# Optimization experiments

Hardware: AMD Instinct MI355X
Metric: run time of the kernel (lower is better)

The kernel has to match this reference:

```python
import jax, jax.numpy as jnp
import numpy as np

EPS = 1e-12  # matches torch F.normalize eps

def _l2norm(x):
    n = jnp.linalg.norm(x, axis=-1, keepdims=True)
    return x / jnp.maximum(n, EPS)

def setup_inputs() -> dict:
    key = jax.random.key(0)
    k1, k2, k3, k4, k5 = jax.random.split(key, 5)
    B, S, D, V, N = 8, 512, 128, 100000, 2048
    query_embeddings = jax.random.normal(k1, (B, S, D), dtype=jnp.float32)
    key_embeddings = jax.random.normal(k2, (V, D), dtype=jnp.float32)
    batch_idx = jax.random.randint(k3, (N, 1), 0, B)
    seq_idx = jax.random.randint(k4, (N, 1), 0, S)
    label_locations = jnp.concatenate([batch_idx, seq_idx], axis=1).astype(jnp.int64)
    labels = jax.random.randint(k5, (N,), 0, V).astype(jnp.int64)
    return {"query_embeddings": query_embeddings, "key_embeddings": key_embeddings,
            "label_locations": label_locations, "labels": labels}

def reference(query_embeddings, key_embeddings, label_locations, labels):
    # gather supervised positions: [N, D]
    q = query_embeddings[label_locations[:, 0], label_locations[:, 1]]
    q = _l2norm(q)
    k = _l2norm(key_embeddings)
    logits = jnp.einsum('nd,vd->nv', q, k)  # [N, V]
    # mean-reduced softmax cross entropy
    logz = jax.nn.logsumexp(logits, axis=-1)  # [N]
    tgt = jnp.take_along_axis(logits, labels[:, None], axis=-1)[:, 0]
    return jnp.mean(logz - tgt)
```

## Files before the change

### kernel.cpp

```cpp
#include <hip/hip_runtime.h>
#include <hip/hip_bf16.h>

typedef __attribute__((ext_vector_type(8))) short short8;
typedef __attribute__((ext_vector_type(4))) short short4v;
typedef __attribute__((ext_vector_type(4))) float f32x4;

namespace {
constexpr int D    = 128;
constexpr int SEQ  = 512;
constexpr int NV   = 100000;
constexpr int NN   = 2048;
constexpr int KC   = 64;
constexpr int CHUNK_B = KC * D * 2;
constexpr int CPS     = 25;
constexpr int NSLICE  = 63;
constexpr int MBLKS   = 8;
constexpr int GRID    = MBLKS * NSLICE;
constexpr float LOG2E = 1.4426950408889634f;
constexpr float EPSN  = 1e-12f;
}

__global__ __launch_bounds__(256)
void prep_kernel(const float* __restrict__ qemb,
                 const float* __restrict__ kemb,
                 const int*   __restrict__ loc,
                 const int*   __restrict__ labels,
                 __hip_bfloat16* __restrict__ Kn,
                 __hip_bfloat16* __restrict__ Qn,
                 float* __restrict__ tgt,
                 float* __restrict__ sums,
                 unsigned int* __restrict__ counter)
{
    const int gid = blockIdx.x * blockDim.x + threadIdx.x;
    if (gid < NN) sums[gid] = 0.f;
    if (gid == NN) *counter = 0u;

    const int gw   = gid >> 6;
    const int lane = threadIdx.x & 63;
    const int half = lane >> 5;
    const int l32  = lane & 31;
    const int row  = gw * 2 + half;
    if (row >= NV + NN) return;

    if (row < NV) {
        const float* src = kemb + (size_t)row * D;
        float4 v = *(const float4*)(src + l32 * 4);
        float ss = v.x * v.x + v.y * v.y + v.z * v.z + v.w * v.w;
        #pragma unroll
        for (int m = 1; m < 32; m <<= 1) ss += __shfl_xor(ss, m);
        float inv = 1.0f / fmaxf(sqrtf(ss), EPSN);
        union { __hip_bfloat162 h2[2]; short4v s4; } u;
        u.h2[0].x = __float2bfloat16(v.x * inv);
        u.h2[0].y = __float2bfloat16(v.y * inv);
        u.h2[1].x = __float2bfloat16(v.z * inv);
        u.h2[1].y = __float2bfloat16(v.w * inv);
        *(short4v*)((char*)(Kn + (size_t)row * D) + l32 * 8) = u.s4;
    } else {
        const int n = row - NV;
        const int b = loc[2 * n], s = loc[2 * n + 1];
        const float* q = qemb + ((size_t)b * SEQ + s) * D;
        const float* k = kemb + (size_t)labels[n] * D;
        float4 qv = *(const float4*)(q + l32 * 4);
        float4 kv = *(const float4*)(k + l32 * 4);
        float qq = qv.x * qv.x + qv.y * qv.y + qv.z * qv.z + qv.w * qv.w;
        float kk = kv.x * kv.x + kv.y * kv.y + kv.z * kv.z + kv.w * kv.w;
        float qk = qv.x * kv.x + qv.y * kv.y + qv.z * kv.z + qv.w * kv.w;
        #pragma unroll
        for (int m = 1; m < 32; m <<= 1) {
            qq += __shfl_xor(qq, m);
            kk += __shfl_xor(kk, m);
            qk += __shfl_xor(qk, m);
        }
        float invq = 1.0f / fmaxf(sqrtf(qq), EPSN);
        float scl  = LOG2E * invq;
        union { __hip_bfloat162 h2[2]; short4v s4; } u;
        u.h2[0].x = __float2bfloat16(qv.x * scl);
        u.h2[0].y = __float2bfloat16(qv.y * scl);
        u.h2[1].x = __float2bfloat16(qv.z * scl);
        u.h2[1].y = __float2bfloat16(qv.w * scl);
        *(short4v*)((char*)(Qn + (size_t)n * D) + l32 * 8) = u.s4;
        if (l32 == 0)
            tgt[n] = qk * invq / fmaxf(sqrtf(kk), EPSN);
    }
}

__global__ __launch_bounds__(256, 2)
void lse_main(const __hip_bfloat16* __restrict__ Kn,
              const __hip_bfloat16* __restrict__ Qn,
              const float* __restrict__ tgt,
              float* __restrict__ sums,
              unsigned int* __restrict__ counter,
              float* __restrict__ out)
{
    __shared__ char lds[4 * CHUNK_B];
    const int tid  = threadIdx.x;
    const int lane = tid & 63;
    const int lr   = lane & 15;
    const int lh   = lane >> 4;
    const int w    = tid >> 6;

    const int bid = blockIdx.x;
    const int lin = (bid & 7) * NSLICE + (bid >> 3);
    const int slice = lin >> 3;
    const int mblk  = lin & 7;

    const int chunk0 = slice * CPS;
    const int m0 = mblk * 256 + w * 64;
    const char* kbase = (const char*)Kn;

    auto stage = [&](int c, int bi) {
        const int keybase = (chunk0 + c) * KC;
        #pragma unroll
        for (int r = 0; r < 4; ++r) {
            const int i   = w * 4 + r;
            const int kic = i * 4 + lh;
            const int key = min(keybase + kic, NV - 1);
            const int sb  = (lr ^ (kic & 7)) << 4;
            const char* g = kbase + (size_t)key * 256 + sb;
            const char* l = lds + bi * CHUNK_B + i * 1024;
            __builtin_amdgcn_global_load_lds(
                (const __attribute__((address_space(1))) void*)g,
                (__attribute__((address_space(3))) void*)l, 16, 0, 0);
        }
    };

    stage(0, 0); stage(1, 1); stage(2, 2);

    short8 qf[4][4];
    #pragma unroll
    for (int rg = 0; rg < 4; ++rg)
        #pragma unroll
        for (int ds = 0; ds < 4; ++ds)
            qf[rg][ds] = *(const short8*)((const short*)Qn +
                          (size_t)(m0 + rg * 16 + lr) * D + ds * 32 + lh * 8);

    float rowsum[4][4] = {};
    __syncthreads();

    for (int c = 0; c < CPS; ++c) {
        if (c + 3 < CPS) stage(c + 3, (c + 3) & 3);

        const char* buf = lds + (c & 3) * CHUNK_B;
        const int vbase = (chunk0 + c) * KC;
        const bool full = (vbase + KC <= NV);
        #pragma unroll
        for (int kg = 0; kg < 4; ++kg) {
            const int kic = kg * 16 + lr;
            const int rx  = (kic & 7) << 4;
            f32x4 acc[4] = {{0,0,0,0},{0,0,0,0},{0,0,0,0},{0,0,0,0}};
            #pragma unroll
            for (int ds2 = 0; ds2 < 4; ++ds2) {
                short8 bf = *(const short8*)(buf +
                              ((kic * 256 + ds2 * 64 + lh * 16) ^ rx));
                #pragma unroll
                for (int rg = 0; rg < 4; ++rg)
                    acc[rg] = __builtin_amdgcn_mfma_f32_16x16x32_bf16(
                                  qf[rg][ds2], bf, acc[rg], 0, 0, 0);
            }
            if (full) {
                #pragma unroll
                for (int rg = 0; rg < 4; ++rg)
                    #pragma unroll
                    for (int j = 0; j < 4; ++j)
                        rowsum[rg][j] += __builtin_amdgcn_exp2f(acc[rg][j]);
            } else {
                const bool ok = (vbase + kic) < NV;
                #pragma unroll
                for (int rg = 0; rg < 4; ++rg)
                    #pragma unroll
                    for (int j = 0; j < 4; ++j)
                        rowsum[rg][j] += ok ? __builtin_amdgcn_exp2f(acc[rg][j]) : 0.f;
            }
        }
        if (c < CPS - 3) {
            asm volatile("s_waitcnt vmcnt(8)" ::: "memory");
            __builtin_amdgcn_s_barrier();
            asm volatile("" ::: "memory");
        } else if (c == CPS - 3) {
            asm volatile("s_waitcnt vmcnt(4)" ::: "memory");
            __builtin_amdgcn_s_barrier();
            asm volatile("" ::: "memory");
        } else if (c == CPS - 2) {
            asm volatile("s_waitcnt vmcnt(0)" ::: "memory");
            __builtin_amdgcn_s_barrier();
            asm volatile("" ::: "memory");
        }
    }

    #pragma unroll
    for (int rg = 0; rg < 4; ++rg)
        #pragma unroll
        for (int j = 0; j < 4; ++j) {
            float v = rowsum[rg][j];
            v += __shfl_xor(v, 1);
            v += __shfl_xor(v, 2);
            v += __shfl_xor(v, 4);
            v += __shfl_xor(v, 8);
            if (lr == 0)
                atomicAdd(&sums[m0 + rg * 16 + lh * 4 + j], v);
        }

    __threadfence();
    __syncthreads();
    __shared__ int ticket_s;
    if (tid == 0) ticket_s = (int)atomicAdd(counter, 1u);
    __syncthreads();
    if (ticket_s == GRID - 1) {
        __threadfence();
        __shared__ float wsum[4];
        float acc = 0.f;
        for (int n = tid; n < NN; n += 256) {
            float sv = __hip_atomic_load(&sums[n], __ATOMIC_RELAXED,
                                         __HIP_MEMORY_SCOPE_AGENT);
            acc += logf(sv) - tgt[n];
        }
        #pragma unroll
        for (int m = 1; m < 64; m <<= 1) acc += __shfl_xor(acc, m);
        if ((tid & 63) == 0) wsum[tid >> 6] = acc;
        __syncthreads();
        if (tid == 0)
            out[0] = (wsum[0] + wsum[1] + wsum[2] + wsum[3]) / (float)NN;
    }
}

extern "C" void kernel_launch(void* const* d_in, const int* in_sizes, int n_in,
                              void* d_out, int out_size, void* d_ws, size_t ws_size,
                              hipStream_t stream)
{
    const float* qemb   = (const float*)d_in[0];
    const float* kemb   = (const float*)d_in[1];
    const int*   loc    = (const int*)d_in[2];
    const int*   labels = (const int*)d_in[3];
    float* out = (float*)d_out;

    char* ws = (char*)d_ws;
    __hip_bfloat16* Kn = (__hip_bfloat16*)ws;
    size_t off = (size_t)NV * D * 2;
    __hip_bfloat16* Qn = (__hip_bfloat16*)(ws + off);
    off += (size_t)NN * D * 2;
    float* sums = (float*)(ws + off); off += (size_t)NN * 4;
    float* tgt  = (float*)(ws + off); off += (size_t)NN * 4;
    unsigned int* counter = (unsigned int*)(ws + off);

    {
        int waves  = (NV + NN + 1) / 2;
        int blocks = (waves + 3) / 4;
        prep_kernel<<<blocks, 256, 0, stream>>>(qemb, kemb, loc, labels,
                                                Kn, Qn, tgt, sums, counter);
    }
    lse_main<<<GRID, 256, 0, stream>>>(Kn, Qn, tgt, sums, counter, out);
}
```

Baseline: 186.1 us.

## Widen LSE blocks to 512 threads, interleave key chunks, grid-stride prep

The main kernel now uses 512-thread blocks covering 512 query rows each, so four M-blocks replace eight and each staged key chunk is reused by twice as many queries. Key chunks are assigned to slices with a stride of NSLICE instead of contiguously, and the block-to-XCD mapping is rebalanced for the uneven 500-block grid. The prep kernel switches to a fixed 2048-block grid-stride loop. The aim is to halve K reloads from L2/HBM. The risk is that `launch_bounds(512,4)` caps VGPRs tightly while the Q fragments alone need many registers, which could cause spills.

```diff
diff --git a/kernel.cpp b/kernel.cpp
--- a/kernel.cpp
+++ b/kernel.cpp
@@ -12,9 +12,10 @@
 constexpr int NN   = 2048;
 constexpr int KC   = 64;
 constexpr int CHUNK_B = KC * D * 2;
-constexpr int CPS     = 25;
-constexpr int NSLICE  = 63;
-constexpr int MBLKS   = 8;
+constexpr int NCHUNK  = 1563;
+constexpr int CPS     = 13;
+constexpr int NSLICE  = 125;
+constexpr int MBLKS   = 4;
 constexpr int GRID    = MBLKS * NSLICE;
 constexpr float LOG2E = 1.4426950408889634f;
 constexpr float EPSN  = 1e-12f;
@@ -31,60 +32,64 @@
                  float* __restrict__ sums,
                  unsigned int* __restrict__ counter)
 {
-    const int gid = blockIdx.x * blockDim.x + threadIdx.x;
-    if (gid < NN) sums[gid] = 0.f;
-    if (gid == NN) *counter = 0u;
-
-    const int gw   = gid >> 6;
-    const int lane = threadIdx.x & 63;
+    const int tid  = threadIdx.x;
+    const int gid0 = blockIdx.x * 256 + tid;
+    if (gid0 < NN) sums[gid0] = 0.f;
+    if (gid0 == NN) *counter = 0u;
+
+    const int lane = tid & 63;
     const int half = lane >> 5;
     const int l32  = lane & 31;
-    const int row  = gw * 2 + half;
-    if (row >= NV + NN) return;
-
-    if (row < NV) {
-        const float* src = kemb + (size_t)row * D;
-        float4 v = *(const float4*)(src + l32 * 4);
-        float ss = v.x * v.x + v.y * v.y + v.z * v.z + v.w * v.w;
-        #pragma unroll
-        for (int m = 1; m < 32; m <<= 1) ss += __shfl_xor(ss, m);
-        float inv = 1.0f / fmaxf(sqrtf(ss), EPSN);
-        union { __hip_bfloat162 h2[2]; short4v s4; } u;
-        u.h2[0].x = __float2bfloat16(v.x * inv);
-        u.h2[0].y = __float2bfloat16(v.y * inv);
-        u.h2[1].x = __float2bfloat16(v.z * inv);
-        u.h2[1].y = __float2bfloat16(v.w * inv);
-        *(short4v*)((char*)(Kn + (size_t)row * D) + l32 * 8) = u.s4;
-    } else {
-        const int n = row - NV;
-        const int b = loc[2 * n], s = loc[2 * n + 1];
-        const float* q = qemb + ((size_t)b * SEQ + s) * D;
-        const float* k = kemb + (size_t)labels[n] * D;
-        float4 qv = *(const float4*)(q + l32 * 4);
-        float4 kv = *(const float4*)(k + l32 * 4);
-        float qq = qv.x * qv.x + qv.y * qv.y + qv.z * qv.z + qv.w * qv.w;
-        float kk = kv.x * kv.x + kv.y * kv.y + kv.z * kv.z + kv.w * kv.w;
-        float qk = qv.x * kv.x + qv.y * kv.y + qv.z * kv.z + qv.w * kv.w;
-        #pragma unroll
-        for (int m = 1; m < 32; m <<= 1) {
-            qq += __shfl_xor(qq, m);
-            kk += __shfl_xor(kk, m);
-            qk += __shfl_xor(qk, m);
-        }
-        float invq = 1.0f / fmaxf(sqrtf(qq), EPSN);
-        float scl  = LOG2E * invq;
-        union { __hip_bfloat162 h2[2]; short4v s4; } u;
-        u.h2[0].x = __float2bfloat16(qv.x * scl);
-        u.h2[0].y = __float2bfloat16(qv.y * scl);
-        u.h2[1].x = __float2bfloat16(qv.z * scl);
-        u.h2[1].y = __float2bfloat16(qv.w * scl);
-        *(short4v*)((char*)(Qn + (size_t)n * D) + l32 * 8) = u.s4;
-        if (l32 == 0)
-            tgt[n] = qk * invq / fmaxf(sqrtf(kk), EPSN);
+    const int wv0  = gid0 >> 6;
+    const int nwv  = (gridDim.x * 256) >> 6;
+
+    for (int wv = wv0; wv * 2 < NV + NN; wv += nwv) {
+        const int row = wv * 2 + half;
+
+        if (row < NV) {
+            const float* src = kemb + (size_t)row * D;
+            float4 v = *(const float4*)(src + l32 * 4);
+            float ss = v.x * v.x + v.y * v.y + v.z * v.z + v.w * v.w;
+            #pragma unroll
+            for (int m = 1; m < 32; m <<= 1) ss += __shfl_xor(ss, m);
+            float inv = 1.0f / fmaxf(sqrtf(ss), EPSN);
+            union { __hip_bfloat162 h2[2]; short4v s4; } u;
+            u.h2[0].x = __float2bfloat16(v.x * inv);
+            u.h2[0].y = __float2bfloat16(v.y * inv);
+            u.h2[1].x = __float2bfloat16(v.z * inv);
+            u.h2[1].y = __float2bfloat16(v.w * inv);
+            *(short4v*)((char*)(Kn + (size_t)row * D) + l32 * 8) = u.s4;
+        } else {
+            const int n = row - NV;
+            const int b = loc[2 * n], s = loc[2 * n + 1];
+            const float* q = qemb + ((size_t)b * SEQ + s) * D;
+            const float* k = kemb + (size_t)labels[n] * D;
+            float4 qv = *(const float4*)(q + l32 * 4);
+            float4 kv = *(const float4*)(k + l32 * 4);
+            float qq = qv.x * qv.x + qv.y * qv.y + qv.z * qv.z + qv.w * qv.w;
+            float kk = kv.x * kv.x + kv.y * kv.y + kv.z * kv.z + kv.w * kv.w;
+            float qk = qv.x * kv.x + qv.y * kv.y + qv.z * kv.z + qv.w * kv.w;
+            #pragma unroll
+            for (int m = 1; m < 32; m <<= 1) {
+                qq += __shfl_xor(qq, m);
+                kk += __shfl_xor(kk, m);
+                qk += __shfl_xor(qk, m);
+            }
+            float invq = 1.0f / fmaxf(sqrtf(qq), EPSN);
+            float scl  = LOG2E * invq;
+            union { __hip_bfloat162 h2[2]; short4v s4; } u;
+            u.h2[0].x = __float2bfloat16(qv.x * scl);
+            u.h2[0].y = __float2bfloat16(qv.y * scl);
+            u.h2[1].x = __float2bfloat16(qv.z * scl);
+            u.h2[1].y = __float2bfloat16(qv.w * scl);
+            *(short4v*)((char*)(Qn + (size_t)n * D) + l32 * 8) = u.s4;
+            if (l32 == 0)
+                tgt[n] = qk * invq / fmaxf(sqrtf(kk), EPSN);
+        }
     }
 }
 
-__global__ __launch_bounds__(256, 2)
+__global__ __launch_bounds__(512, 4)
 void lse_main(const __hip_bfloat16* __restrict__ Kn,
               const __hip_bfloat16* __restrict__ Qn,
               const float* __restrict__ tgt,
@@ -100,19 +105,21 @@
     const int w    = tid >> 6;
 
     const int bid = blockIdx.x;
-    const int lin = (bid & 7) * NSLICE + (bid >> 3);
-    const int slice = lin >> 3;
-    const int mblk  = lin & 7;
-
-    const int chunk0 = slice * CPS;
-    const int m0 = mblk * 256 + w * 64;
+    const int xcd = bid & 7, idx = bid >> 3;
+    const int base = (xcd < 4) ? xcd * 63 : 252 + (xcd - 4) * 62;
+    const int lin  = base + idx;
+    const int slice = lin >> 2;
+    const int mblk  = lin & 3;
+
+    const int m0 = mblk * 512 + w * 64;
     const char* kbase = (const char*)Kn;
 
     auto stage = [&](int c, int bi) {
-        const int keybase = (chunk0 + c) * KC;
-        #pragma unroll
-        for (int r = 0; r < 4; ++r) {
-            const int i   = w * 4 + r;
+        const int chunk = slice + c * NSLICE;
+        const int keybase = chunk * KC;
+        #pragma unroll
+        for (int r = 0; r < 2; ++r) {
+            const int i   = w * 2 + r;
             const int kic = i * 4 + lh;
             const int key = min(keybase + kic, NV - 1);
             const int sb  = (lr ^ (kic & 7)) << 4;
@@ -141,7 +148,7 @@
         if (c + 3 < CPS) stage(c + 3, (c + 3) & 3);
 
         const char* buf = lds + (c & 3) * CHUNK_B;
-        const int vbase = (chunk0 + c) * KC;
+        const int vbase = (slice + c * NSLICE) * KC;
         const bool full = (vbase + KC <= NV);
         #pragma unroll
         for (int kg = 0; kg < 4; ++kg) {
@@ -173,11 +180,11 @@
             }
         }
         if (c < CPS - 3) {
-            asm volatile("s_waitcnt vmcnt(8)" ::: "memory");
+            asm volatile("s_waitcnt vmcnt(4)" ::: "memory");
             __builtin_amdgcn_s_barrier();
             asm volatile("" ::: "memory");
         } else if (c == CPS - 3) {
-            asm volatile("s_waitcnt vmcnt(4)" ::: "memory");
+            asm volatile("s_waitcnt vmcnt(2)" ::: "memory");
             __builtin_amdgcn_s_barrier();
             asm volatile("" ::: "memory");
         } else if (c == CPS - 2) {
@@ -207,9 +214,9 @@
     __syncthreads();
     if (ticket_s == GRID - 1) {
         __threadfence();
-        __shared__ float wsum[4];
+        __shared__ float wsum[8];
         float acc = 0.f;
-        for (int n = tid; n < NN; n += 256) {
+        for (int n = tid; n < NN; n += 512) {
             float sv = __hip_atomic_load(&sums[n], __ATOMIC_RELAXED,
                                          __HIP_MEMORY_SCOPE_AGENT);
             acc += logf(sv) - tgt[n];
@@ -218,8 +225,12 @@
         for (int m = 1; m < 64; m <<= 1) acc += __shfl_xor(acc, m);
         if ((tid & 63) == 0) wsum[tid >> 6] = acc;
         __syncthreads();
-        if (tid == 0)
-            out[0] = (wsum[0] + wsum[1] + wsum[2] + wsum[3]) / (float)NN;
+        if (tid == 0) {
+            float t = 0.f;
+            #pragma unroll
+            for (int i = 0; i < 8; ++i) t += wsum[i];
+            out[0] = t / (float)NN;
+        }
     }
 }
 
@@ -242,11 +253,7 @@
     float* tgt  = (float*)(ws + off); off += (size_t)NN * 4;
     unsigned int* counter = (unsigned int*)(ws + off);
 
-    {
-        int waves  = (NV + NN + 1) / 2;
-        int blocks = (waves + 3) / 4;
-        prep_kernel<<<blocks, 256, 0, stream>>>(qemb, kemb, loc, labels,
-                                                Kn, Qn, tgt, sums, counter);
-    }
-    lse_main<<<GRID, 256, 0, stream>>>(Kn, Qn, tgt, sums, counter, out);
-}
+    prep_kernel<<<2048, 256, 0, stream>>>(qemb, kemb, loc, labels,
+                                          Kn, Qn, tgt, sums, counter);
+    lse_main<<<GRID, 512, 0, stream>>>(Kn, Qn, tgt, sums, counter, out);
+}
```

Measured after the change: 434.2 us. +133.4%, slower.

## Shrink LDS ring to three buffers, use finer key slices, grid-stride prep

Applied to the files above, without the earlier changes.

The main kernel's LDS ring drops from four to three 16KB buffers with a prefetch distance of two, lowering shared memory per block so more blocks can be resident. Keys are split into 92 slices of 17 chunks instead of 63 of 25, giving more blocks for load balance, and a per-slice chunk count handles the ragged last slice. The prep kernel becomes a grid-stride loop over a fixed 2048-block grid instead of one wave per row pair. The shallower prefetch may expose more memory latency per chunk.

```diff
diff --git a/kernel.cpp b/kernel.cpp
--- a/kernel.cpp
+++ b/kernel.cpp
@@ -12,8 +12,9 @@
 constexpr int NN   = 2048;
 constexpr int KC   = 64;
 constexpr int CHUNK_B = KC * D * 2;
-constexpr int CPS     = 25;
-constexpr int NSLICE  = 63;
+constexpr int NCHUNK  = 1563;
+constexpr int CPS     = 17;
+constexpr int NSLICE  = 92;
 constexpr int MBLKS   = 8;
 constexpr int GRID    = MBLKS * NSLICE;
 constexpr float LOG2E = 1.4426950408889634f;
@@ -31,56 +32,60 @@
                  float* __restrict__ sums,
                  unsigned int* __restrict__ counter)
 {
-    const int gid = blockIdx.x * blockDim.x + threadIdx.x;
-    if (gid < NN) sums[gid] = 0.f;
-    if (gid == NN) *counter = 0u;
-
-    const int gw   = gid >> 6;
-    const int lane = threadIdx.x & 63;
+    const int tid  = threadIdx.x;
+    const int gid0 = blockIdx.x * 256 + tid;
+    if (gid0 < NN) sums[gid0] = 0.f;
+    if (gid0 == NN) *counter = 0u;
+
+    const int lane = tid & 63;
     const int half = lane >> 5;
     const int l32  = lane & 31;
-    const int row  = gw * 2 + half;
-    if (row >= NV + NN) return;
-
-    if (row < NV) {
-        const float* src = kemb + (size_t)row * D;
-        float4 v = *(const float4*)(src + l32 * 4);
-        float ss = v.x * v.x + v.y * v.y + v.z * v.z + v.w * v.w;
-        #pragma unroll
-        for (int m = 1; m < 32; m <<= 1) ss += __shfl_xor(ss, m);
-        float inv = 1.0f / fmaxf(sqrtf(ss), EPSN);
-        union { __hip_bfloat162 h2[2]; short4v s4; } u;
-        u.h2[0].x = __float2bfloat16(v.x * inv);
-        u.h2[0].y = __float2bfloat16(v.y * inv);
-        u.h2[1].x = __float2bfloat16(v.z * inv);
-        u.h2[1].y = __float2bfloat16(v.w * inv);
-        *(short4v*)((char*)(Kn + (size_t)row * D) + l32 * 8) = u.s4;
-    } else {
-        const int n = row - NV;
-        const int b = loc[2 * n], s = loc[2 * n + 1];
-        const float* q = qemb + ((size_t)b * SEQ + s) * D;
-        const float* k = kemb + (size_t)labels[n] * D;
-        float4 qv = *(const float4*)(q + l32 * 4);
-        float4 kv = *(const float4*)(k + l32 * 4);
-        float qq = qv.x * qv.x + qv.y * qv.y + qv.z * qv.z + qv.w * qv.w;
-        float kk = kv.x * kv.x + kv.y * kv.y + kv.z * kv.z + kv.w * kv.w;
-        float qk = qv.x * kv.x + qv.y * kv.y + qv.z * kv.z + qv.w * kv.w;
-        #pragma unroll
-        for (int m = 1; m < 32; m <<= 1) {
-            qq += __shfl_xor(qq, m);
-            kk += __shfl_xor(kk, m);
-            qk += __shfl_xor(qk, m);
-        }
-        float invq = 1.0f / fmaxf(sqrtf(qq), EPSN);
-        float scl  = LOG2E * invq;
-        union { __hip_bfloat162 h2[2]; short4v s4; } u;
-        u.h2[0].x = __float2bfloat16(qv.x * scl);
-        u.h2[0].y = __float2bfloat16(qv.y * scl);
-        u.h2[1].x = __float2bfloat16(qv.z * scl);
-        u.h2[1].y = __float2bfloat16(qv.w * scl);
-        *(short4v*)((char*)(Qn + (size_t)n * D) + l32 * 8) = u.s4;
-        if (l32 == 0)
-            tgt[n] = qk * invq / fmaxf(sqrtf(kk), EPSN);
+    const int wv0  = gid0 >> 6;
+    const int nwv  = (gridDim.x * 256) >> 6;
+
+    for (int wv = wv0; wv * 2 < NV + NN; wv += nwv) {
+        const int row = wv * 2 + half;
+
+        if (row < NV) {
+            const float* src = kemb + (size_t)row * D;
+            float4 v = *(const float4*)(src + l32 * 4);
+            float ss = v.x * v.x + v.y * v.y + v.z * v.z + v.w * v.w;
+            #pragma unroll
+            for (int m = 1; m < 32; m <<= 1) ss += __shfl_xor(ss, m);
+            float inv = 1.0f / fmaxf(sqrtf(ss), EPSN);
+            union { __hip_bfloat162 h2[2]; short4v s4; } u;
+            u.h2[0].x = __float2bfloat16(v.x * inv);
+            u.h2[0].y = __float2bfloat16(v.y * inv);
+            u.h2[1].x = __float2bfloat16(v.z * inv);
+            u.h2[1].y = __float2bfloat16(v.w * inv);
+            *(short4v*)((char*)(Kn + (size_t)row * D) + l32 * 8) = u.s4;
+        } else {
+            const int n = row - NV;
+            const int b = loc[2 * n], s = loc[2 * n + 1];
+            const float* q = qemb + ((size_t)b * SEQ + s) * D;
+            const float* k = kemb + (size_t)labels[n] * D;
+            float4 qv = *(const float4*)(q + l32 * 4);
+            float4 kv = *(const float4*)(k + l32 * 4);
+            float qq = qv.x * qv.x + qv.y * qv.y + qv.z * qv.z + qv.w * qv.w;
+            float kk = kv.x * kv.x + kv.y * kv.y + kv.z * kv.z + kv.w * kv.w;
+            float qk = qv.x * kv.x + qv.y * kv.y + qv.z * kv.z + qv.w * kv.w;
+            #pragma unroll
+            for (int m = 1; m < 32; m <<= 1) {
+                qq += __shfl_xor(qq, m);
+                kk += __shfl_xor(kk, m);
+                qk += __shfl_xor(qk, m);
+            }
+            float invq = 1.0f / fmaxf(sqrtf(qq), EPSN);
+            float scl  = LOG2E * invq;
+            union { __hip_bfloat162 h2[2]; short4v s4; } u;
+            u.h2[0].x = __float2bfloat16(qv.x * scl);
+            u.h2[0].y = __float2bfloat16(qv.y * scl);
+            u.h2[1].x = __float2bfloat16(qv.z * scl);
+            u.h2[1].y = __float2bfloat16(qv.w * scl);
+            *(short4v*)((char*)(Qn + (size_t)n * D) + l32 * 8) = u.s4;
+            if (l32 == 0)
+                tgt[n] = qk * invq / fmaxf(sqrtf(kk), EPSN);
+        }
     }
 }
 
@@ -92,7 +97,7 @@
               unsigned int* __restrict__ counter,
               float* __restrict__ out)
 {
-    __shared__ char lds[4 * CHUNK_B];
+    __shared__ char lds[3 * CHUNK_B];
     const int tid  = threadIdx.x;
     const int lane = tid & 63;
     const int lr   = lane & 15;
@@ -105,6 +110,7 @@
     const int mblk  = lin & 7;
 
     const int chunk0 = slice * CPS;
+    const int nch = min(CPS, NCHUNK - chunk0);
     const int m0 = mblk * 256 + w * 64;
     const char* kbase = (const char*)Kn;
 
@@ -124,7 +130,7 @@
         }
     };
 
-    stage(0, 0); stage(1, 1); stage(2, 2);
+    stage(0, 0); stage(1, 1);
 
     short8 qf[4][4];
     #pragma unroll
@@ -137,10 +143,10 @@
     float rowsum[4][4] = {};
     __syncthreads();
 
-    for (int c = 0; c < CPS; ++c) {
-        if (c + 3 < CPS) stage(c + 3, (c + 3) & 3);
-
-        const char* buf = lds + (c & 3) * CHUNK_B;
+    for (int c = 0; c < nch; ++c) {
+        if (c + 2 < nch) stage(c + 2, (c + 2) % 3);
+
+        const char* buf = lds + (c % 3) * CHUNK_B;
         const int vbase = (chunk0 + c) * KC;
         const bool full = (vbase + KC <= NV);
         #pragma unroll
@@ -172,15 +178,11 @@
                         rowsum[rg][j] += ok ? __builtin_amdgcn_exp2f(acc[rg][j]) : 0.f;
             }
         }
-        if (c < CPS - 3) {
-            asm volatile("s_waitcnt vmcnt(8)" ::: "memory");
-            __builtin_amdgcn_s_barrier();
-            asm volatile("" ::: "memory");
-        } else if (c == CPS - 3) {
+        if (c + 2 < nch) {
             asm volatile("s_waitcnt vmcnt(4)" ::: "memory");
             __builtin_amdgcn_s_barrier();
             asm volatile("" ::: "memory");
-        } else if (c == CPS - 2) {
+        } else if (c + 2 == nch) {
             asm volatile("s_waitcnt vmcnt(0)" ::: "memory");
             __builtin_amdgcn_s_barrier();
             asm volatile("" ::: "memory");
@@ -242,11 +244,7 @@
     float* tgt  = (float*)(ws + off); off += (size_t)NN * 4;
     unsigned int* counter = (unsigned int*)(ws + off);
 
-    {
-        int waves  = (NV + NN + 1) / 2;
-        int blocks = (waves + 3) / 4;
-        prep_kernel<<<blocks, 256, 0, stream>>>(qemb, kemb, loc, labels,
-                                                Kn, Qn, tgt, sums, counter);
-    }
+    prep_kernel<<<2048, 256, 0, stream>>>(qemb, kemb, loc, labels,
+                                          Kn, Qn, tgt, sums, counter);
     lse_main<<<GRID, 256, 0, stream>>>(Kn, Qn, tgt, sums, counter, out);
 }
```

New measurement: 208.8 us. +12.2%, slower.
